# Kernel optimization log

Measured on AMD Instinct MI355X. Metric: run time of the kernel, lower is better.

The kernel has to match this reference:

```python
import jax, jax.numpy as jnp
import numpy as np

N = 50000          # num nodes
E = 800000         # num edges (before self-loops)
F_IN = 128         # num_node_features
HEADS = 8          # num_heads (layer 1)
F_HEAD = 16        # features_per_head
N_CLASSES = 32     # num_classes (layer 2, heads=1)
NEG_SLOPE = 0.2    # PyG GATConv default LeakyReLU slope


def setup_inputs() -> dict:
    key = jax.random.key(0)
    ks = jax.random.split(key, 9)
    x = jax.random.normal(ks[0], (N, F_IN), jnp.float32)
    src = jax.random.randint(ks[1], (E,), 0, N, dtype=jnp.int32)
    dst = jax.random.randint(ks[2], (E,), 0, N, dtype=jnp.int32)
    # layer 1 params
    W1 = jax.random.normal(ks[3], (F_IN, HEADS * F_HEAD), jnp.float32) / np.sqrt(F_IN).astype(np.float32)
    a_src1 = jax.random.normal(ks[4], (HEADS, F_HEAD), jnp.float32) * 0.1
    a_dst1 = jax.random.normal(ks[5], (HEADS, F_HEAD), jnp.float32) * 0.1
    b1 = jnp.zeros((HEADS * F_HEAD,), jnp.float32)  # bias_init = zeros_
    # layer 2 params (heads=1)
    W2 = jax.random.normal(ks[6], (HEADS * F_HEAD, N_CLASSES), jnp.float32) / np.sqrt(HEADS * F_HEAD).astype(np.float32)
    a_src2 = jax.random.normal(ks[7], (1, N_CLASSES), jnp.float32) * 0.1
    a_dst2 = jax.random.normal(ks[8], (1, N_CLASSES), jnp.float32) * 0.1
    b2 = jnp.zeros((N_CLASSES,), jnp.float32)
    return {"x": x, "src": src, "dst": dst,
            "W1": W1, "a_src1": a_src1, "a_dst1": a_dst1, "b1": b1,
            "W2": W2, "a_src2": a_src2, "a_dst2": a_dst2, "b2": b2}


def gat_conv(x, src, dst, W, a_src, a_dst, b, heads, feat):
    """PyG-style GATConv (concat=True, add_self_loops=True)."""
    h = (x @ W).reshape(N, heads, feat)                 # [N,H,F]
    al_src = jnp.sum(h * a_src, axis=-1)                # [N,H]
    al_dst = jnp.sum(h * a_dst, axis=-1)                # [N,H]
    loop = jnp.arange(N, dtype=src.dtype)
    s = jnp.concatenate([src, loop])                    # [E+N]
    d = jnp.concatenate([dst, loop])                    # [E+N]
    e = jax.nn.leaky_relu(al_src[s] + al_dst[d], NEG_SLOPE)   # [E+N,H]
    # numerically stable softmax over edges grouped by dst node
    m = jax.ops.segment_max(e, d, num_segments=N)       # [N,H]
    ex = jnp.exp(e - m[d])
    denom = jax.ops.segment_sum(ex, d, num_segments=N)  # [N,H]
    alpha = ex / denom[d]                               # [E+N,H]
    out = jax.ops.segment_sum(alpha[:, :, None] * h[s], d, num_segments=N)  # [N,H,F]
    return out.reshape(N, heads * feat) + b


def reference(x, src, dst, W1, a_src1, a_dst1, b1, W2, a_src2, a_dst2, b2):
    h = gat_conv(x, src, dst, W1, a_src1, a_dst1, b1, HEADS, F_HEAD)
    h = jax.nn.elu(h)
    h = gat_conv(h, src, dst, W2, a_src2, a_dst2, b2, 1, N_CLASSES)
    return jax.nn.log_softmax(h, axis=1)
```

## Files before the change

kernel.cpp:

```cpp
#include <hip/hip_runtime.h>

#define N_NODES   50000
#define N_EDGES   800000
#define NEG_SLOPE 0.2f
#define NBKT      256
#define NPB       196
#define EPB       3125
#define CAP       4096
#define G1BLK     782

__device__ __forceinline__ float leaky(float x) {
    return x > 0.f ? x : x * NEG_SLOPE;
}

__device__ __forceinline__ unsigned short f2bf(float f) {
    unsigned int u = __float_as_uint(f);
    unsigned int r = (u + 0x7FFFu + ((u >> 16) & 1u)) >> 16;
    return (unsigned short)r;
}

__device__ __forceinline__ unsigned int pack2bf(float a, float b) {
    return (unsigned int)f2bf(a) | ((unsigned int)f2bf(b) << 16);
}

__device__ __forceinline__ float2 bf2f2(unsigned int p) {
    return make_float2(__uint_as_float(p << 16),
                       __uint_as_float(p & 0xFFFF0000u));
}

__device__ __forceinline__ float4 up4(uint2 q) {
    return make_float4(__uint_as_float(q.x << 16),
                       __uint_as_float(q.x & 0xFFFF0000u),
                       __uint_as_float(q.y << 16),
                       __uint_as_float(q.y & 0xFFFF0000u));
}

__device__ __forceinline__ void fma4(float4& acc, const float4 a,
                                     const float4 w0, const float4 w1,
                                     const float4 w2, const float4 w3) {
    acc.x = fmaf(a.x, w0.x, fmaf(a.y, w1.x, fmaf(a.z, w2.x, fmaf(a.w, w3.x, acc.x))));
    acc.y = fmaf(a.x, w0.y, fmaf(a.y, w1.y, fmaf(a.z, w2.y, fmaf(a.w, w3.y, acc.y))));
    acc.z = fmaf(a.x, w0.z, fmaf(a.y, w1.z, fmaf(a.z, w2.z, fmaf(a.w, w3.z, acc.z))));
    acc.w = fmaf(a.x, w0.w, fmaf(a.y, w1.w, fmaf(a.z, w2.w, fmaf(a.w, w3.w, acc.w))));
}

__device__ __forceinline__ float dot4(const float4 a, const float4 b) {
    return a.x * b.x + a.y * b.y + a.z * b.z + a.w * b.w;
}

__global__ __launch_bounds__(256) void k_bin_gemm1(
    const int* __restrict__ src, const int* __restrict__ dst,
    int* __restrict__ cursor_g, unsigned int* __restrict__ binned,
    const float* __restrict__ x, const float* __restrict__ W1,
    const float* __restrict__ a_src, const float* __restrict__ a_dst,
    unsigned short* __restrict__ h1b, float* __restrict__ al_src,
    float* __restrict__ al_dst)
{
    __shared__ __align__(16) unsigned char smem[49152];
    const int tid = threadIdx.x;

    if (blockIdx.x < NBKT) {
        int* dstc = (int*)smem;
        int* cnt  = (int*)(smem + 12512);
        int* cur  = (int*)(smem + 13536);
        const int blk = blockIdx.x;
        const int e0  = blk * EPB;
        cnt[tid] = 0;
        __syncthreads();
        for (int j = tid; j < EPB; j += 256) {
            int d = dst[e0 + j];
            dstc[j] = d;
            atomicAdd(&cnt[d / NPB], 1);
        }
        __syncthreads();
        const int c = cnt[tid];
        int base = c ? atomicAdd(&cursor_g[tid], c) : 0;
        cur[tid] = tid * CAP + base;
        __syncthreads();
        for (int j = tid; j < EPB; j += 256) {
            int d   = dstc[j];
            int bkt = d / NPB;
            int dl  = d - bkt * NPB;
            int pos = atomicAdd(&cur[bkt], 1);
            binned[pos] = (unsigned int)src[e0 + j] | ((unsigned int)dl << 18);
        }
        return;
    }

    uint2* xs = (uint2*)smem;
    uint2* ws = (uint2*)(smem + 16384);
    const int bid  = (int)blockIdx.x - NBKT;
    const int row0 = bid * 64;
    const int tc   = tid & 31;
    const int tr   = tid >> 5;
    const float4* x4  = (const float4*)x;
    const float4* W14 = (const float4*)W1;

    #pragma unroll
    for (int p = 0; p < 8; ++p) {
        int i = tid + p * 256;
        int r = i >> 5, g = i & 31;
        int gr = row0 + r; if (gr > N_NODES - 1) gr = N_NODES - 1;
        float4 v = x4[gr * 32 + g];
        xs[r * 32 + g] = make_uint2(pack2bf(v.x, v.y), pack2bf(v.z, v.w));
    }
    #pragma unroll
    for (int p = 0; p < 16; ++p) {
        int i = tid + p * 256;
        int k = i >> 5, cg = i & 31;
        float4 v = W14[k * 32 + cg];
        ws[k * 32 + cg] = make_uint2(pack2bf(v.x, v.y), pack2bf(v.z, v.w));
    }
    __syncthreads();

    float4 acc[8];
    #pragma unroll
    for (int i = 0; i < 8; ++i) acc[i] = make_float4(0.f, 0.f, 0.f, 0.f);

    for (int k4 = 0; k4 < 32; ++k4) {
        float4 a4[8];
        #pragma unroll
        for (int i = 0; i < 8; ++i)
            a4[i] = up4(xs[(tr * 8 + i) * 32 + k4]);
        #pragma unroll
        for (int kk = 0; kk < 4; ++kk) {
            float4 w = up4(ws[(k4 * 4 + kk) * 32 + tc]);
            #pragma unroll
            for (int i = 0; i < 8; ++i) {
                float a = (kk == 0) ? a4[i].x : (kk == 1) ? a4[i].y
                        : (kk == 2) ? a4[i].z : a4[i].w;
                acc[i].x = fmaf(a, w.x, acc[i].x);
                acc[i].y = fmaf(a, w.y, acc[i].y);
                acc[i].z = fmaf(a, w.z, acc[i].z);
                acc[i].w = fmaf(a, w.w, acc[i].w);
            }
        }
    }

    const int head = tc >> 2;
    const float4 as4 = ((const float4*)a_src)[tc];
    const float4 ad4 = ((const float4*)a_dst)[tc];
    #pragma unroll
    for (int i = 0; i < 8; ++i) {
        int r = row0 + tr * 8 + i;
        float s = dot4(acc[i], as4);
        float d = dot4(acc[i], ad4);
        s += __shfl_xor(s, 1); s += __shfl_xor(s, 2);
        d += __shfl_xor(d, 1); d += __shfl_xor(d, 2);
        if (r < N_NODES) {
            ((uint2*)h1b)[r * 32 + tc] =
                make_uint2(pack2bf(acc[i].x, acc[i].y), pack2bf(acc[i].z, acc[i].w));
            if ((tc & 3) == 0) {
                al_src[r * 8 + head] = s;
                al_dst[r * 8 + head] = d;
            }
        }
    }
}

__global__ __launch_bounds__(256) void k_csr_fine(const unsigned int* __restrict__ binned,
                                                  const int* __restrict__ cursor_g,
                                                  int* __restrict__ row_beg,
                                                  int* __restrict__ row_end,
                                                  int* __restrict__ csr) {
    __shared__ int cnt[256];
    __shared__ int sc[256];
    __shared__ int cur[256];
    const int b = blockIdx.x, tid = threadIdx.x;
    const int start = b * CAP;
    const int nE    = cursor_g[b];
    cnt[tid] = 0;
    __syncthreads();
    for (int j = tid; j < nE; j += 256)
        atomicAdd(&cnt[(binned[start + j] >> 18) & 255], 1);
    __syncthreads();
    const int v = cnt[tid];
    sc[tid] = v;
    __syncthreads();
    for (int off = 1; off < 256; off <<= 1) {
        int add = (tid >= off) ? sc[tid - off] : 0;
        __syncthreads();
        sc[tid] += add;
        __syncthreads();
    }
    const int excl = sc[tid] - v;
    cur[tid] = excl;
    const int node = b * NPB + tid;
    if (tid < NPB && node < N_NODES) {
        row_beg[node] = start + excl;
        row_end[node] = start + excl + v;
    }
    __syncthreads();
    for (int j = tid; j < nE; j += 256) {
        unsigned int p = binned[start + j];
        int dl  = (p >> 18) & 255;
        int pos = start + atomicAdd(&cur[dl], 1);
        csr[pos] = (int)(p & 0x3FFFFu);
    }
}

__global__ __launch_bounds__(256) void k_agg1(
    const unsigned short* __restrict__ h1b, const float* __restrict__ al_src,
    const float* __restrict__ al_dst, const int* __restrict__ row_beg,
    const int* __restrict__ row_end, const int* __restrict__ csr_src,
    const float* __restrict__ b1, float* __restrict__ h2)
{
    const int n = blockIdx.x * 4 + (threadIdx.x >> 6);
    const int l    = threadIdx.x & 63;
    const int slot = l >> 4;
    const int f2   = l & 15;
    const int head = f2 >> 1;
    const uint4* h1q = (const uint4*)h1b;

    const float alD = al_dst[n * 8 + head];
    float denom = 0.f;
    float acc[8];
    #pragma unroll
    for (int i = 0; i < 8; ++i) acc[i] = 0.f;

    if (slot == 0) {
        float w = __expf(leaky(al_src[n * 8 + head] + alD));
        uint4 q = h1q[n * 16 + f2];
        float2 v0 = bf2f2(q.x), v1 = bf2f2(q.y), v2 = bf2f2(q.z), v3 = bf2f2(q.w);
        denom = w;
        acc[0] = w * v0.x; acc[1] = w * v0.y; acc[2] = w * v1.x; acc[3] = w * v1.y;
        acc[4] = w * v2.x; acc[5] = w * v2.y; acc[6] = w * v3.x; acc[7] = w * v3.y;
    }

    const int beg = row_beg[n], end = row_end[n];
    int j = beg + slot;
    for (; j + 4 < end; j += 8) {
        int sa = csr_src[j];
        int sb = csr_src[j + 4];
        float ala = al_src[sa * 8 + head];
        float alb = al_src[sb * 8 + head];
        uint4 qa = h1q[sa * 16 + f2];
        uint4 qb = h1q[sb * 16 + f2];
        float wa = __expf(leaky(ala + alD));
        float wb = __expf(leaky(alb + alD));
        denom += wa + wb;
        float2 v;
        v = bf2f2(qa.x); acc[0] = fmaf(wa, v.x, acc[0]); acc[1] = fmaf(wa, v.y, acc[1]);
        v = bf2f2(qa.y); acc[2] = fmaf(wa, v.x, acc[2]); acc[3] = fmaf(wa, v.y, acc[3]);
        v = bf2f2(qa.z); acc[4] = fmaf(wa, v.x, acc[4]); acc[5] = fmaf(wa, v.y, acc[5]);
        v = bf2f2(qa.w); acc[6] = fmaf(wa, v.x, acc[6]); acc[7] = fmaf(wa, v.y, acc[7]);
        v = bf2f2(qb.x); acc[0] = fmaf(wb, v.x, acc[0]); acc[1] = fmaf(wb, v.y, acc[1]);
        v = bf2f2(qb.y); acc[2] = fmaf(wb, v.x, acc[2]); acc[3] = fmaf(wb, v.y, acc[3]);
        v = bf2f2(qb.z); acc[4] = fmaf(wb, v.x, acc[4]); acc[5] = fmaf(wb, v.y, acc[5]);
        v = bf2f2(qb.w); acc[6] = fmaf(wb, v.x, acc[6]); acc[7] = fmaf(wb, v.y, acc[7]);
    }
    if (j < end) {
        int s = csr_src[j];
        float w = __expf(leaky(al_src[s * 8 + head] + alD));
        uint4 q = h1q[s * 16 + f2];
        denom += w;
        float2 v;
        v = bf2f2(q.x); acc[0] = fmaf(w, v.x, acc[0]); acc[1] = fmaf(w, v.y, acc[1]);
        v = bf2f2(q.y); acc[2] = fmaf(w, v.x, acc[2]); acc[3] = fmaf(w, v.y, acc[3]);
        v = bf2f2(q.z); acc[4] = fmaf(w, v.x, acc[4]); acc[5] = fmaf(w, v.y, acc[5]);
        v = bf2f2(q.w); acc[6] = fmaf(w, v.x, acc[6]); acc[7] = fmaf(w, v.y, acc[7]);
    }

    #pragma unroll
    for (int i = 0; i < 8; ++i) {
        acc[i] += __shfl_xor(acc[i], 16);
        acc[i] += __shfl_xor(acc[i], 32);
    }
    denom += __shfl_xor(denom, 16);
    denom += __shfl_xor(denom, 32);

    if (slot == 0) {
        const float4 bA = ((const float4*)b1)[f2 * 2];
        const float4 bB = ((const float4*)b1)[f2 * 2 + 1];
        float inv = 1.f / denom;
        float o[8];
        o[0] = acc[0] * inv + bA.x; o[1] = acc[1] * inv + bA.y;
        o[2] = acc[2] * inv + bA.z; o[3] = acc[3] * inv + bA.w;
        o[4] = acc[4] * inv + bB.x; o[5] = acc[5] * inv + bB.y;
        o[6] = acc[6] * inv + bB.z; o[7] = acc[7] * inv + bB.w;
        #pragma unroll
        for (int i = 0; i < 8; ++i) o[i] = o[i] > 0.f ? o[i] : expm1f(o[i]);
        ((float4*)h2)[n * 32 + f2 * 2]     = make_float4(o[0], o[1], o[2], o[3]);
        ((float4*)h2)[n * 32 + f2 * 2 + 1] = make_float4(o[4], o[5], o[6], o[7]);
    }
}

__global__ __launch_bounds__(128) void k_gemm2(
    const float* __restrict__ h2, const float* __restrict__ W2,
    const float* __restrict__ a_src, const float* __restrict__ a_dst,
    unsigned short* __restrict__ t2b, float* __restrict__ al_src,
    float* __restrict__ al_dst)
{
    __shared__ float4 xs4[64 * 32];
    __shared__ float4 ws4[128 * 8];
    const int tid  = threadIdx.x;
    const int row0 = (int)blockIdx.x * 64;
    const int tc   = tid & 7;
    const int tr   = tid >> 3;
    const float4* h24 = (const float4*)h2;
    const float4* W24 = (const float4*)W2;

    #pragma unroll
    for (int p = 0; p < 8; ++p) {
        int i = tid + p * 128;
        ws4[i] = W24[i];
    }
    #pragma unroll
    for (int p = 0; p < 16; ++p) {
        int i = tid + p * 128;
        int r = i >> 5, k4 = i & 31;
        int gr = row0 + r; if (gr > N_NODES - 1) gr = N_NODES - 1;
        xs4[r * 32 + (k4 ^ ((r >> 2) & 7))] = h24[gr * 32 + k4];
    }
    __syncthreads();

    float4 acc[4];
    #pragma unroll
    for (int i = 0; i < 4; ++i) acc[i] = make_float4(0.f, 0.f, 0.f, 0.f);
    const int sw = tr & 7;
    #pragma unroll 2
    for (int k4 = 0; k4 < 32; ++k4) {
        float4 w0 = ws4[(4 * k4 + 0) * 8 + tc];
        float4 w1 = ws4[(4 * k4 + 1) * 8 + tc];
        float4 w2 = ws4[(4 * k4 + 2) * 8 + tc];
        float4 w3 = ws4[(4 * k4 + 3) * 8 + tc];
        const int kk = k4 ^ sw;
        #pragma unroll
        for (int i = 0; i < 4; ++i) {
            float4 a = xs4[(4 * tr + i) * 32 + kk];
            fma4(acc[i], a, w0, w1, w2, w3);
        }
    }

    const float4 as4 = ((const float4*)a_src)[tc];
    const float4 ad4 = ((const float4*)a_dst)[tc];
    #pragma unroll
    for (int i = 0; i < 4; ++i) {
        int r = row0 + 4 * tr + i;
        if (r < N_NODES) {
            ((ushort4*)t2b)[r * 8 + tc] =
                make_ushort4(f2bf(acc[i].x), f2bf(acc[i].y),
                             f2bf(acc[i].z), f2bf(acc[i].w));
            float s = dot4(acc[i], as4);
            float d = dot4(acc[i], ad4);
            s += __shfl_xor(s, 1); s += __shfl_xor(s, 2); s += __shfl_xor(s, 4);
            d += __shfl_xor(d, 1); d += __shfl_xor(d, 2); d += __shfl_xor(d, 4);
            if (tc == 0) {
                al_src[r] = s;
                al_dst[r] = d;
            }
        }
    }
}

__global__ __launch_bounds__(256) void k_agg2(
    const unsigned short* __restrict__ t2b, const float* __restrict__ al_src,
    const float* __restrict__ al_dst, const int* __restrict__ row_beg,
    const int* __restrict__ row_end, const int* __restrict__ csr_src,
    const float* __restrict__ b2, float* __restrict__ out)
{
    const int n = blockIdx.x * 4 + (threadIdx.x >> 6);
    const int l = threadIdx.x & 63;
    const int slot = l >> 3;
    const int f4   = l & 7;
    const uint2* t2u = (const uint2*)t2b;

    const float alD = al_dst[n];
    float denom = 0.f;
    float4 acc = make_float4(0.f, 0.f, 0.f, 0.f);
    if (slot == 0) {
        float w = __expf(leaky(al_src[n] + alD));
        uint2 q = t2u[n * 8 + f4];
        float2 v0 = bf2f2(q.x), v1 = bf2f2(q.y);
        denom = w;
        acc = make_float4(w * v0.x, w * v0.y, w * v1.x, w * v1.y);
    }
    const int beg = row_beg[n], end = row_end[n];
    int j = beg + slot;
    for (; j + 8 < end; j += 16) {
        int sa = csr_src[j];
        int sb = csr_src[j + 8];
        float ala = al_src[sa];
        float alb = al_src[sb];
        uint2 qa = t2u[sa * 8 + f4];
        uint2 qb = t2u[sb * 8 + f4];
        float wa = __expf(leaky(ala + alD));
        float wb = __expf(leaky(alb + alD));
        denom += wa + wb;
        float2 v;
        v = bf2f2(qa.x); acc.x = fmaf(wa, v.x, acc.x); acc.y = fmaf(wa, v.y, acc.y);
        v = bf2f2(qa.y); acc.z = fmaf(wa, v.x, acc.z); acc.w = fmaf(wa, v.y, acc.w);
        v = bf2f2(qb.x); acc.x = fmaf(wb, v.x, acc.x); acc.y = fmaf(wb, v.y, acc.y);
        v = bf2f2(qb.y); acc.z = fmaf(wb, v.x, acc.z); acc.w = fmaf(wb, v.y, acc.w);
    }
    if (j < end) {
        int s = csr_src[j];
        float w = __expf(leaky(al_src[s] + alD));
        uint2 q = t2u[s * 8 + f4];
        denom += w;
        float2 v;
        v = bf2f2(q.x); acc.x = fmaf(w, v.x, acc.x); acc.y = fmaf(w, v.y, acc.y);
        v = bf2f2(q.y); acc.z = fmaf(w, v.x, acc.z); acc.w = fmaf(w, v.y, acc.w);
    }
    #pragma unroll
    for (int off = 8; off <= 32; off <<= 1) {
        acc.x += __shfl_xor(acc.x, off); acc.y += __shfl_xor(acc.y, off);
        acc.z += __shfl_xor(acc.z, off); acc.w += __shfl_xor(acc.w, off);
        denom += __shfl_xor(denom, off);
    }

    const float4 bb = ((const float4*)b2)[f4];
    float inv = 1.f / denom;
    float o0 = acc.x * inv + bb.x;
    float o1 = acc.y * inv + bb.y;
    float o2 = acc.z * inv + bb.z;
    float o3 = acc.w * inv + bb.w;
    float m = fmaxf(fmaxf(o0, o1), fmaxf(o2, o3));
    for (int off = 1; off <= 4; off <<= 1) m = fmaxf(m, __shfl_xor(m, off));
    float ssum = __expf(o0 - m) + __expf(o1 - m) + __expf(o2 - m) + __expf(o3 - m);
    for (int off = 1; off <= 4; off <<= 1) ssum += __shfl_xor(ssum, off);
    float lg = m + __logf(ssum);
    if (slot == 0)
        ((float4*)out)[n * 8 + f4] = make_float4(o0 - lg, o1 - lg, o2 - lg, o3 - lg);
}

extern "C" void kernel_launch(void* const* d_in, const int* in_sizes, int n_in,
                              void* d_out, int out_size, void* d_ws, size_t ws_size,
                              hipStream_t stream) {
    const float* x      = (const float*)d_in[0];
    const int*   src    = (const int*)d_in[1];
    const int*   dst    = (const int*)d_in[2];
    const float* W1     = (const float*)d_in[3];
    const float* a_src1 = (const float*)d_in[4];
    const float* a_dst1 = (const float*)d_in[5];
    const float* b1     = (const float*)d_in[6];
    const float* W2     = (const float*)d_in[7];
    const float* a_src2 = (const float*)d_in[8];
    const float* a_dst2 = (const float*)d_in[9];
    const float* b2     = (const float*)d_in[10];
    float* out = (float*)d_out;

    char* ws = (char*)d_ws;
    size_t off = 0;
    auto alloc = [&](size_t bytes) {
        void* p = ws + off;
        off += (bytes + 255) & ~(size_t)255;
        return p;
    };
    unsigned short* h1b = (unsigned short*)alloc((size_t)N_NODES * 128 * 2);
    float*          h2  = (float*)alloc((size_t)N_NODES * 128 * 4);
    unsigned short* t2b = (unsigned short*)alloc((size_t)N_NODES * 32 * 2);
    float* alS1    = (float*)alloc((size_t)N_NODES * 8 * 4);
    float* alD1    = (float*)alloc((size_t)N_NODES * 8 * 4);
    float* alS2    = (float*)alloc((size_t)N_NODES * 4);
    float* alD2    = (float*)alloc((size_t)N_NODES * 4);
    int*   row_beg = (int*)alloc((size_t)N_NODES * 4);
    int*   row_end = (int*)alloc((size_t)N_NODES * 4);
    int*   csr     = (int*)alloc((size_t)NBKT * CAP * 4);
    unsigned int* binned = (unsigned int*)alloc((size_t)NBKT * CAP * 4);
    int*   cursor  = (int*)alloc((size_t)NBKT * 4);
    (void)ws_size; (void)in_sizes; (void)n_in; (void)out_size;

    const int row_tiles = (N_NODES + 63) / 64;

    hipMemsetAsync(cursor, 0, (size_t)NBKT * 4, stream);
    k_bin_gemm1<<<NBKT + G1BLK, 256, 0, stream>>>(
        src, dst, cursor, binned,
        x, W1, a_src1, a_dst1, h1b, alS1, alD1);
    k_csr_fine<<<NBKT, 256, 0, stream>>>(binned, cursor, row_beg, row_end, csr);
    k_agg1<<<N_NODES / 4, 256, 0, stream>>>(h1b, alS1, alD1, row_beg, row_end, csr, b1, h2);
    k_gemm2<<<row_tiles, 128, 0, stream>>>(h2, W2, a_src2, a_dst2, t2b, alS2, alD2);
    k_agg2<<<N_NODES / 4, 256, 0, stream>>>(t2b, alS2, alD2, row_beg, row_end, csr, b2, out);
}
```

Before: 217.5 us.

## Fuse layer-2 GEMM and attention logits into layer-1 aggregation kernel

Merges the layer-1 aggregation kernel with the layer-2 dense projection. Each wave writes its ELU output row to shared memory and multiplies it by W2, which every block copies into LDS. It then emits the bf16 projected features and both attention logits directly. This removes the fp32 h2 round trip through global memory and one kernel launch. In exchange, each block reloads the full W2 matrix into LDS and uses more shared memory, which may reduce occupancy in the gather-heavy aggregation.

```diff
diff --git a/kernel.cpp b/kernel.cpp
--- a/kernel.cpp
+++ b/kernel.cpp
@@ -33,15 +33,6 @@
                        __uint_as_float(q.x & 0xFFFF0000u),
                        __uint_as_float(q.y << 16),
                        __uint_as_float(q.y & 0xFFFF0000u));
-}
-
-__device__ __forceinline__ void fma4(float4& acc, const float4 a,
-                                     const float4 w0, const float4 w1,
-                                     const float4 w2, const float4 w3) {
-    acc.x = fmaf(a.x, w0.x, fmaf(a.y, w1.x, fmaf(a.z, w2.x, fmaf(a.w, w3.x, acc.x))));
-    acc.y = fmaf(a.x, w0.y, fmaf(a.y, w1.y, fmaf(a.z, w2.y, fmaf(a.w, w3.y, acc.y))));
-    acc.z = fmaf(a.x, w0.z, fmaf(a.y, w1.z, fmaf(a.z, w2.z, fmaf(a.w, w3.z, acc.z))));
-    acc.w = fmaf(a.x, w0.w, fmaf(a.y, w1.w, fmaf(a.z, w2.w, fmaf(a.w, w3.w, acc.w))));
 }
 
 __device__ __forceinline__ float dot4(const float4 a, const float4 b) {
@@ -199,18 +190,29 @@
     }
 }
 
-__global__ __launch_bounds__(256) void k_agg1(
+__global__ __launch_bounds__(256) void k_agg1g2(
     const unsigned short* __restrict__ h1b, const float* __restrict__ al_src,
     const float* __restrict__ al_dst, const int* __restrict__ row_beg,
     const int* __restrict__ row_end, const int* __restrict__ csr_src,
-    const float* __restrict__ b1, float* __restrict__ h2)
+    const float* __restrict__ b1, const float* __restrict__ W2,
+    const float* __restrict__ a_src2, const float* __restrict__ a_dst2,
+    unsigned short* __restrict__ t2b, float* __restrict__ alS2,
+    float* __restrict__ alD2)
 {
-    const int n = blockIdx.x * 4 + (threadIdx.x >> 6);
-    const int l    = threadIdx.x & 63;
+    __shared__ float w2s[128 * 32];
+    __shared__ float h2row[4][128];
+    const int tid  = threadIdx.x;
+    const int wv   = tid >> 6;
+    const int n    = blockIdx.x * 4 + wv;
+    const int l    = tid & 63;
     const int slot = l >> 4;
     const int f2   = l & 15;
     const int head = f2 >> 1;
     const uint4* h1q = (const uint4*)h1b;
+
+    #pragma unroll
+    for (int p = 0; p < 16; ++p)
+        w2s[tid + p * 256] = W2[tid + p * 256];
 
     const float alD = al_dst[n * 8 + head];
     float denom = 0.f;
@@ -269,7 +271,7 @@
     denom += __shfl_xor(denom, 16);
     denom += __shfl_xor(denom, 32);
 
-    if (slot == 0) {
+    {
         const float4 bA = ((const float4*)b1)[f2 * 2];
         const float4 bB = ((const float4*)b1)[f2 * 2 + 1];
         float inv = 1.f / denom;
@@ -280,76 +282,33 @@
         o[6] = acc[6] * inv + bB.z; o[7] = acc[7] * inv + bB.w;
         #pragma unroll
         for (int i = 0; i < 8; ++i) o[i] = o[i] > 0.f ? o[i] : expm1f(o[i]);
-        ((float4*)h2)[n * 32 + f2 * 2]     = make_float4(o[0], o[1], o[2], o[3]);
-        ((float4*)h2)[n * 32 + f2 * 2 + 1] = make_float4(o[4], o[5], o[6], o[7]);
-    }
-}
-
-__global__ __launch_bounds__(128) void k_gemm2(
-    const float* __restrict__ h2, const float* __restrict__ W2,
-    const float* __restrict__ a_src, const float* __restrict__ a_dst,
-    unsigned short* __restrict__ t2b, float* __restrict__ al_src,
-    float* __restrict__ al_dst)
-{
-    __shared__ float4 xs4[64 * 32];
-    __shared__ float4 ws4[128 * 8];
-    const int tid  = threadIdx.x;
-    const int row0 = (int)blockIdx.x * 64;
-    const int tc   = tid & 7;
-    const int tr   = tid >> 3;
-    const float4* h24 = (const float4*)h2;
-    const float4* W24 = (const float4*)W2;
-
-    #pragma unroll
-    for (int p = 0; p < 8; ++p) {
-        int i = tid + p * 128;
-        ws4[i] = W24[i];
-    }
-    #pragma unroll
-    for (int p = 0; p < 16; ++p) {
-        int i = tid + p * 128;
-        int r = i >> 5, k4 = i & 31;
-        int gr = row0 + r; if (gr > N_NODES - 1) gr = N_NODES - 1;
-        xs4[r * 32 + (k4 ^ ((r >> 2) & 7))] = h24[gr * 32 + k4];
-    }
-    __syncthreads();
-
-    float4 acc[4];
-    #pragma unroll
-    for (int i = 0; i < 4; ++i) acc[i] = make_float4(0.f, 0.f, 0.f, 0.f);
-    const int sw = tr & 7;
-    #pragma unroll 2
-    for (int k4 = 0; k4 < 32; ++k4) {
-        float4 w0 = ws4[(4 * k4 + 0) * 8 + tc];
-        float4 w1 = ws4[(4 * k4 + 1) * 8 + tc];
-        float4 w2 = ws4[(4 * k4 + 2) * 8 + tc];
-        float4 w3 = ws4[(4 * k4 + 3) * 8 + tc];
-        const int kk = k4 ^ sw;
-        #pragma unroll
-        for (int i = 0; i < 4; ++i) {
-            float4 a = xs4[(4 * tr + i) * 32 + kk];
-            fma4(acc[i], a, w0, w1, w2, w3);
+        if (slot == 0) {
+            *(float4*)&h2row[wv][f2 * 8]     = make_float4(o[0], o[1], o[2], o[3]);
+            *(float4*)&h2row[wv][f2 * 8 + 4] = make_float4(o[4], o[5], o[6], o[7]);
         }
     }
-
-    const float4 as4 = ((const float4*)a_src)[tc];
-    const float4 ad4 = ((const float4*)a_dst)[tc];
-    #pragma unroll
-    for (int i = 0; i < 4; ++i) {
-        int r = row0 + 4 * tr + i;
-        if (r < N_NODES) {
-            ((ushort4*)t2b)[r * 8 + tc] =
-                make_ushort4(f2bf(acc[i].x), f2bf(acc[i].y),
-                             f2bf(acc[i].z), f2bf(acc[i].w));
-            float s = dot4(acc[i], as4);
-            float d = dot4(acc[i], ad4);
-            s += __shfl_xor(s, 1); s += __shfl_xor(s, 2); s += __shfl_xor(s, 4);
-            d += __shfl_xor(d, 1); d += __shfl_xor(d, 2); d += __shfl_xor(d, 4);
-            if (tc == 0) {
-                al_src[r] = s;
-                al_dst[r] = d;
-            }
-        }
+    __syncthreads();
+
+    const int c  = l & 31;
+    const int kh = l >> 5;
+    const float* hr = h2row[wv];
+    float sum = 0.f;
+    #pragma unroll 8
+    for (int k = kh * 64; k < kh * 64 + 64; ++k)
+        sum = fmaf(hr[k], w2s[k * 32 + c], sum);
+    sum += __shfl_xor(sum, 32);
+
+    if (l < 32) t2b[n * 32 + c] = f2bf(sum);
+    float s2 = sum * a_src2[c];
+    float d2 = sum * a_dst2[c];
+    #pragma unroll
+    for (int off = 1; off <= 16; off <<= 1) {
+        s2 += __shfl_xor(s2, off);
+        d2 += __shfl_xor(d2, off);
+    }
+    if (l == 0) {
+        alS2[n] = s2;
+        alD2[n] = d2;
     }
 }
 
@@ -448,7 +407,6 @@
         return p;
     };
     unsigned short* h1b = (unsigned short*)alloc((size_t)N_NODES * 128 * 2);
-    float*          h2  = (float*)alloc((size_t)N_NODES * 128 * 4);
     unsigned short* t2b = (unsigned short*)alloc((size_t)N_NODES * 32 * 2);
     float* alS1    = (float*)alloc((size_t)N_NODES * 8 * 4);
     float* alD1    = (float*)alloc((size_t)N_NODES * 8 * 4);
@@ -461,14 +419,13 @@
     int*   cursor  = (int*)alloc((size_t)NBKT * 4);
     (void)ws_size; (void)in_sizes; (void)n_in; (void)out_size;
 
-    const int row_tiles = (N_NODES + 63) / 64;
-
     hipMemsetAsync(cursor, 0, (size_t)NBKT * 4, stream);
     k_bin_gemm1<<<NBKT + G1BLK, 256, 0, stream>>>(
         src, dst, cursor, binned,
         x, W1, a_src1, a_dst1, h1b, alS1, alD1);
     k_csr_fine<<<NBKT, 256, 0, stream>>>(binned, cursor, row_beg, row_end, csr);
-    k_agg1<<<N_NODES / 4, 256, 0, stream>>>(h1b, alS1, alD1, row_beg, row_end, csr, b1, h2);
-    k_gemm2<<<row_tiles, 128, 0, stream>>>(h2, W2, a_src2, a_dst2, t2b, alS2, alD2);
+    k_agg1g2<<<N_NODES / 4, 256, 0, stream>>>(
+        h1b, alS1, alD1, row_beg, row_end, csr,
+        b1, W2, a_src2, a_dst2, t2b, alS2, alD2);
     k_agg2<<<N_NODES / 4, 256, 0, stream>>>(t2b, alS2, alD2, row_beg, row_end, csr, b2, out);
 }
```

Result: faster. 212.1 us (-2.5%).
